# Kernel optimization log

Measured on AMD Instinct MI355X. Metric: run time of the kernel, lower is better.

## Reference

```python
import jax, jax.numpy as jnp
import numpy as np

B, N_ELEM, N_NODES, E2 = 4096, 2048, 1024, 4096


def setup_inputs() -> dict:
    key = jax.random.key(0)
    k = jax.random.split(key, 7)
    return {
        "EA": jax.random.normal(k[0], (B, N_ELEM), dtype=jnp.float32),
        "e": jax.random.normal(k[1], (B, N_ELEM), dtype=jnp.float32),
        "q": jax.random.normal(k[2], (B, N_NODES, 2), dtype=jnp.float32),
        "r": jax.random.normal(k[3], (B, N_NODES, 2), dtype=jnp.float32),
        "vecs": jax.random.normal(k[4], (E2, 2), dtype=jnp.float32),
        "node_ids": jax.random.randint(k[5], (E2,), 0, N_NODES, dtype=jnp.int32),
        "elem_ids": jax.random.randint(k[6], (E2,), 0, N_ELEM, dtype=jnp.int32),
    }


def reference(EA, e, q, r, vecs, node_ids, elem_ids):
    # axial_forces = EA * e : [B, N_ELEM]
    axial = EA * e
    # gather per incidence entry and scale by the 2-vector: [B, E2, 2]
    contrib = axial[:, elem_ids][..., None] * vecs[None, :, :]
    n_sample, n_nodes = q.shape[0], q.shape[1]
    # scatter-add contributions into per-node residual: [B, N_NODES, 2]
    residual = jnp.zeros((n_sample, n_nodes, 2), dtype=EA.dtype)
    residual = residual.at[:, node_ids, :].add(contrib)
    residual = residual - q - r
    return jnp.mean(jnp.square(residual))
```

## Files before the change

kernel.cpp:

```cpp
#include <hip/hip_runtime.h>

#define B_SAMPLES 4096
#define N_ELEM    2048
#define N_NODES   1024
#define E2        4096
#define BLOCK     256
#define MBLOCK    512
#define SLOTS     32
#define S         4
#define MAIN_BLOCKS (B_SAMPLES / S)

#define WS_CNT_OFF   0
#define WS_ELL_OFF   4096
#define WS_PART_OFF  (4096 + SLOTS * N_NODES * 16)

__global__ __launch_bounds__(BLOCK) void neq_zero_kernel(
    float4* __restrict__ ell, int* __restrict__ cnt)
{
    const int i = blockIdx.x * BLOCK + threadIdx.x;
    ell[i] = make_float4(0.f, 0.f, 0.f, 0.f);
    if (i < N_NODES) cnt[i] = 0;
}

__global__ __launch_bounds__(BLOCK) void neq_build_kernel(
    const float* __restrict__ vecs, const int* __restrict__ node_ids,
    const int* __restrict__ elem_ids, int* __restrict__ cnt,
    float4* __restrict__ ell)
{
    const int j = blockIdx.x * BLOCK + threadIdx.x;
    int nid = node_ids[j];
    int eid = elem_ids[j];
    float2 v = ((const float2*)vecs)[j];
    int slot = atomicAdd(&cnt[nid], 1);
    if (slot < SLOTS) {
        ell[slot * N_NODES + nid] = make_float4(v.x, v.y, __int_as_float(eid), 0.f);
    }
}

__global__ __launch_bounds__(MBLOCK, 8) void neq_main_kernel(
    const float* __restrict__ EA, const float* __restrict__ e,
    const float* __restrict__ q,  const float* __restrict__ r,
    const int* __restrict__ cnt, const float4* __restrict__ ell,
    float* __restrict__ partial)
{
    __shared__ float4 axial4[N_ELEM];
    __shared__ float red[MBLOCK / 64];

    const int b0 = blockIdx.x * S;
    const int t = threadIdx.x;

#pragma unroll
    for (int i = 0; i < N_ELEM / MBLOCK; ++i) {
        int eid = t + i * MBLOCK;
        float4 p;
        const float* EAp = EA + (size_t)b0 * N_ELEM + eid;
        const float* ep  = e  + (size_t)b0 * N_ELEM + eid;
        p.x = EAp[0 * N_ELEM] * ep[0 * N_ELEM];
        p.y = EAp[1 * N_ELEM] * ep[1 * N_ELEM];
        p.z = EAp[2 * N_ELEM] * ep[2 * N_ELEM];
        p.w = EAp[3 * N_ELEM] * ep[3 * N_ELEM];
        axial4[eid] = p;
    }

    int c0 = min(cnt[t], SLOTS);
    int c1 = min(cnt[t + MBLOCK], SLOTS);
    int kmax = max(c0, c1);
    __syncthreads();

    float accx[2][S] = {};
    float accy[2][S] = {};
    for (int k = 0; k < kmax; ++k) {
        const float4* row = ell + k * N_NODES + t;
#pragma unroll
        for (int i = 0; i < 2; ++i) {
            float4 pk = row[i * MBLOCK];
            int eid = __float_as_int(pk.z);
            float4 ax = axial4[eid];
            accx[i][0] += ax.x * pk.x;  accy[i][0] += ax.x * pk.y;
            accx[i][1] += ax.y * pk.x;  accy[i][1] += ax.y * pk.y;
            accx[i][2] += ax.z * pk.x;  accy[i][2] += ax.z * pk.y;
            accx[i][3] += ax.w * pk.x;  accy[i][3] += ax.w * pk.y;
        }
    }

    float acc = 0.f;
#pragma unroll
    for (int s = 0; s < S; ++s) {
        const float2* q2 = (const float2*)(q + (size_t)(b0 + s) * N_NODES * 2);
        const float2* r2 = (const float2*)(r + (size_t)(b0 + s) * N_NODES * 2);
#pragma unroll
        for (int i = 0; i < 2; ++i) {
            int n = t + i * MBLOCK;
            float2 qv = q2[n];
            float2 rv = r2[n];
            float x = accx[i][s] - qv.x - rv.x;
            float y = accy[i][s] - qv.y - rv.y;
            acc += x * x + y * y;
        }
    }

#pragma unroll
    for (int off = 32; off > 0; off >>= 1)
        acc += __shfl_down(acc, off, 64);
    if ((t & 63) == 0) red[t >> 6] = acc;
    __syncthreads();
    if (t == 0) {
        float s = 0.f;
#pragma unroll
        for (int w = 0; w < MBLOCK / 64; ++w) s += red[w];
        partial[blockIdx.x] = s;
    }
}

__global__ __launch_bounds__(1024) void neq_reduce_kernel(
    const float* __restrict__ partial, float* __restrict__ out)
{
    __shared__ float red[1024 / 64];
    const int t = threadIdx.x;
    float acc = partial[t];
#pragma unroll
    for (int off = 32; off > 0; off >>= 1)
        acc += __shfl_down(acc, off, 64);
    if ((t & 63) == 0) red[t >> 6] = acc;
    __syncthreads();
    if (t == 0) {
        float s = 0.f;
#pragma unroll
        for (int w = 0; w < 1024 / 64; ++w) s += red[w];
        const float inv_n = 1.0f / (float)((size_t)B_SAMPLES * N_NODES * 2);
        out[0] = s * inv_n;
    }
}

extern "C" void kernel_launch(void* const* d_in, const int* in_sizes, int n_in,
                              void* d_out, int out_size, void* d_ws, size_t ws_size,
                              hipStream_t stream) {
    const float* EA       = (const float*)d_in[0];
    const float* e        = (const float*)d_in[1];
    const float* q        = (const float*)d_in[2];
    const float* r        = (const float*)d_in[3];
    const float* vecs     = (const float*)d_in[4];
    const int*   node_ids = (const int*)d_in[5];
    const int*   elem_ids = (const int*)d_in[6];

    char* ws = (char*)d_ws;
    int*    cnt     = (int*)(ws + WS_CNT_OFF);
    float4* ell     = (float4*)(ws + WS_ELL_OFF);
    float*  partial = (float*)(ws + WS_PART_OFF);

    neq_zero_kernel<<<(SLOTS * N_NODES) / BLOCK, BLOCK, 0, stream>>>(ell, cnt);
    neq_build_kernel<<<E2 / BLOCK, BLOCK, 0, stream>>>(
        vecs, node_ids, elem_ids, cnt, ell);
    neq_main_kernel<<<MAIN_BLOCKS, MBLOCK, 0, stream>>>(
        EA, e, q, r, cnt, ell, partial);
    neq_reduce_kernel<<<1, 1024, 0, stream>>>(partial, (float*)d_out);
}
```

Baseline: 162.4 us.

## Halve samples per block, use float4 loads and swizzled float2 shared axial layout

The main kernel now processes 2 samples per block with 256 threads, so there are twice as many blocks, and each thread handles 4 nodes. EA and e are loaded with vectorized float4 reads. The axial values are stored in shared memory as float2 under a swizzled element index, which the build kernel precomputes so the gather maps correctly. This aims to improve global load coalescing, halve shared memory per block and raise occupancy, at the cost of reading the ELL table twice as many times in total.

```diff
diff --git a/kernel.cpp b/kernel.cpp
--- a/kernel.cpp
+++ b/kernel.cpp
@@ -5,14 +5,18 @@
 #define N_NODES   1024
 #define E2        4096
 #define BLOCK     256
-#define MBLOCK    512
+#define MBLOCK    256
 #define SLOTS     32
-#define S         4
+#define S         2
 #define MAIN_BLOCKS (B_SAMPLES / S)
 
 #define WS_CNT_OFF   0
 #define WS_ELL_OFF   4096
 #define WS_PART_OFF  (4096 + SLOTS * N_NODES * 16)
+
+__host__ __device__ __forceinline__ int swz_eid(int eid) {
+    return ((eid & 3) << 9) | (eid >> 2);
+}
 
 __global__ __launch_bounds__(BLOCK) void neq_zero_kernel(
     float4* __restrict__ ell, int* __restrict__ cnt)
@@ -29,7 +33,7 @@
 {
     const int j = blockIdx.x * BLOCK + threadIdx.x;
     int nid = node_ids[j];
-    int eid = elem_ids[j];
+    int eid = swz_eid(elem_ids[j]);
     float2 v = ((const float2*)vecs)[j];
     int slot = atomicAdd(&cnt[nid], 1);
     if (slot < SLOTS) {
@@ -37,50 +41,75 @@
     }
 }
 
+#define GFMA2(ACCX, ACCY, PK) do { \
+    float2 gv = axial2[__float_as_int((PK).z)]; \
+    (ACCX).x += gv.x * (PK).x; (ACCX).y += gv.y * (PK).x; \
+    (ACCY).x += gv.x * (PK).y; (ACCY).y += gv.y * (PK).y; } while (0)
+
 __global__ __launch_bounds__(MBLOCK, 8) void neq_main_kernel(
     const float* __restrict__ EA, const float* __restrict__ e,
     const float* __restrict__ q,  const float* __restrict__ r,
     const int* __restrict__ cnt, const float4* __restrict__ ell,
     float* __restrict__ partial)
 {
-    __shared__ float4 axial4[N_ELEM];
+    __shared__ float2 axial2[N_ELEM];
     __shared__ float red[MBLOCK / 64];
 
     const int b0 = blockIdx.x * S;
     const int t = threadIdx.x;
 
-#pragma unroll
-    for (int i = 0; i < N_ELEM / MBLOCK; ++i) {
-        int eid = t + i * MBLOCK;
-        float4 p;
-        const float* EAp = EA + (size_t)b0 * N_ELEM + eid;
-        const float* ep  = e  + (size_t)b0 * N_ELEM + eid;
-        p.x = EAp[0 * N_ELEM] * ep[0 * N_ELEM];
-        p.y = EAp[1 * N_ELEM] * ep[1 * N_ELEM];
-        p.z = EAp[2 * N_ELEM] * ep[2 * N_ELEM];
-        p.w = EAp[3 * N_ELEM] * ep[3 * N_ELEM];
-        axial4[eid] = p;
+    const float4* EA4 = (const float4*)(EA + (size_t)b0 * N_ELEM);
+    const float4* e4  = (const float4*)(e  + (size_t)b0 * N_ELEM);
+    float4 a00 = EA4[t];
+    float4 a01 = EA4[t + 256];
+    float4 a10 = EA4[512 + t];
+    float4 a11 = EA4[512 + t + 256];
+    float4 m00 = e4[t];
+    float4 m01 = e4[t + 256];
+    float4 m10 = e4[512 + t];
+    float4 m11 = e4[512 + t + 256];
+
+    int n0 = min(cnt[t], SLOTS);
+    int n1 = min(cnt[t + 256], SLOTS);
+    int n2 = min(cnt[t + 512], SLOTS);
+    int n3 = min(cnt[t + 768], SLOTS);
+    int kmax = max(max(n0, n1), max(n2, n3));
+
+    {
+        float4 p0, p1;
+        p0.x = a00.x * m00.x; p0.y = a00.y * m00.y; p0.z = a00.z * m00.z; p0.w = a00.w * m00.w;
+        p1.x = a10.x * m10.x; p1.y = a10.y * m10.y; p1.z = a10.z * m10.z; p1.w = a10.w * m10.w;
+        axial2[t]        = make_float2(p0.x, p1.x);
+        axial2[t + 512]  = make_float2(p0.y, p1.y);
+        axial2[t + 1024] = make_float2(p0.z, p1.z);
+        axial2[t + 1536] = make_float2(p0.w, p1.w);
     }
-
-    int c0 = min(cnt[t], SLOTS);
-    int c1 = min(cnt[t + MBLOCK], SLOTS);
-    int kmax = max(c0, c1);
+    {
+        float4 p0, p1;
+        p0.x = a01.x * m01.x; p0.y = a01.y * m01.y; p0.z = a01.z * m01.z; p0.w = a01.w * m01.w;
+        p1.x = a11.x * m11.x; p1.y = a11.y * m11.y; p1.z = a11.z * m11.z; p1.w = a11.w * m11.w;
+        axial2[t + 256]  = make_float2(p0.x, p1.x);
+        axial2[t + 768]  = make_float2(p0.y, p1.y);
+        axial2[t + 1280] = make_float2(p0.z, p1.z);
+        axial2[t + 1792] = make_float2(p0.w, p1.w);
+    }
     __syncthreads();
 
-    float accx[2][S] = {};
-    float accy[2][S] = {};
+    float2 accx0 = make_float2(0.f, 0.f), accy0 = make_float2(0.f, 0.f);
+    float2 accx1 = make_float2(0.f, 0.f), accy1 = make_float2(0.f, 0.f);
+    float2 accx2 = make_float2(0.f, 0.f), accy2 = make_float2(0.f, 0.f);
+    float2 accx3 = make_float2(0.f, 0.f), accy3 = make_float2(0.f, 0.f);
+
     for (int k = 0; k < kmax; ++k) {
-        const float4* row = ell + k * N_NODES + t;
-#pragma unroll
-        for (int i = 0; i < 2; ++i) {
-            float4 pk = row[i * MBLOCK];
-            int eid = __float_as_int(pk.z);
-            float4 ax = axial4[eid];
-            accx[i][0] += ax.x * pk.x;  accy[i][0] += ax.x * pk.y;
-            accx[i][1] += ax.y * pk.x;  accy[i][1] += ax.y * pk.y;
-            accx[i][2] += ax.z * pk.x;  accy[i][2] += ax.z * pk.y;
-            accx[i][3] += ax.w * pk.x;  accy[i][3] += ax.w * pk.y;
-        }
+        const float4* row = ell + (size_t)k * N_NODES;
+        float4 pk0 = row[t];
+        float4 pk1 = row[t + 256];
+        float4 pk2 = row[t + 512];
+        float4 pk3 = row[t + 768];
+        GFMA2(accx0, accy0, pk0);
+        GFMA2(accx1, accy1, pk1);
+        GFMA2(accx2, accy2, pk2);
+        GFMA2(accx3, accy3, pk3);
     }
 
     float acc = 0.f;
@@ -88,15 +117,19 @@
     for (int s = 0; s < S; ++s) {
         const float2* q2 = (const float2*)(q + (size_t)(b0 + s) * N_NODES * 2);
         const float2* r2 = (const float2*)(r + (size_t)(b0 + s) * N_NODES * 2);
-#pragma unroll
-        for (int i = 0; i < 2; ++i) {
-            int n = t + i * MBLOCK;
-            float2 qv = q2[n];
-            float2 rv = r2[n];
-            float x = accx[i][s] - qv.x - rv.x;
-            float y = accy[i][s] - qv.y - rv.y;
-            acc += x * x + y * y;
-        }
+        float2 qa = q2[t],       ra = r2[t];
+        float2 qb = q2[t + 256], rb = r2[t + 256];
+        float2 qc = q2[t + 512], rc = r2[t + 512];
+        float2 qd = q2[t + 768], rd = r2[t + 768];
+        float ax, ay, x, y;
+        ax = (s == 0) ? accx0.x : accx0.y;  ay = (s == 0) ? accy0.x : accy0.y;
+        x = ax - qa.x - ra.x;  y = ay - qa.y - ra.y;  acc += x * x + y * y;
+        ax = (s == 0) ? accx1.x : accx1.y;  ay = (s == 0) ? accy1.x : accy1.y;
+        x = ax - qb.x - rb.x;  y = ay - qb.y - rb.y;  acc += x * x + y * y;
+        ax = (s == 0) ? accx2.x : accx2.y;  ay = (s == 0) ? accy2.x : accy2.y;
+        x = ax - qc.x - rc.x;  y = ay - qc.y - rc.y;  acc += x * x + y * y;
+        ax = (s == 0) ? accx3.x : accx3.y;  ay = (s == 0) ? accy3.x : accy3.y;
+        x = ax - qd.x - rd.x;  y = ay - qd.y - rd.y;  acc += x * x + y * y;
     }
 
 #pragma unroll
@@ -104,12 +137,7 @@
         acc += __shfl_down(acc, off, 64);
     if ((t & 63) == 0) red[t >> 6] = acc;
     __syncthreads();
-    if (t == 0) {
-        float s = 0.f;
-#pragma unroll
-        for (int w = 0; w < MBLOCK / 64; ++w) s += red[w];
-        partial[blockIdx.x] = s;
-    }
+    if (t == 0) partial[blockIdx.x] = red[0] + red[1] + red[2] + red[3];
 }
 
 __global__ __launch_bounds__(1024) void neq_reduce_kernel(
@@ -117,7 +145,7 @@
 {
     __shared__ float red[1024 / 64];
     const int t = threadIdx.x;
-    float acc = partial[t];
+    float acc = partial[t] + partial[t + 1024];
 #pragma unroll
     for (int off = 32; off > 0; off >>= 1)
         acc += __shfl_down(acc, off, 64);
```

Result: slower. 192.1 us (+18.3%).

## Process eight samples per block with swizzled axial layout and split ELL arrays

Applied to the files above, without the earlier changes.

Each block now handles eight samples instead of four, so every gathered ELL entry (weight and element index) is reused across twice as many samples. Axial forces are loaded as float4 vectors from global memory and stored transposed into two shared arrays, using a swizzled element index precomputed in the build kernel. The ELL table is split into a float2 weight array and an int index array to cut the bytes read per entry. In exchange, shared memory per block doubles to 64KB and the launch-bounds occupancy hint drops from 8 to 4, which lowers occupancy.

```diff
diff --git a/kernel.cpp b/kernel.cpp
--- a/kernel.cpp
+++ b/kernel.cpp
@@ -7,96 +7,166 @@
 #define BLOCK     256
 #define MBLOCK    512
 #define SLOTS     32
-#define S         4
+#define S         8
 #define MAIN_BLOCKS (B_SAMPLES / S)
 
-#define WS_CNT_OFF   0
-#define WS_ELL_OFF   4096
-#define WS_PART_OFF  (4096 + SLOTS * N_NODES * 16)
+#define WS_CNT_OFF    0
+#define WS_ELLW_OFF   4096
+#define WS_ELLID_OFF  (4096 + SLOTS * N_NODES * 8)
+#define WS_PART_OFF   (WS_ELLID_OFF + SLOTS * N_NODES * 4)
+
+__host__ __device__ __forceinline__ int swz_eid(int eid) {
+    return ((eid & 3) << 9) | (eid >> 2);
+}
 
 __global__ __launch_bounds__(BLOCK) void neq_zero_kernel(
-    float4* __restrict__ ell, int* __restrict__ cnt)
+    float2* __restrict__ ellw, int* __restrict__ ellid, int* __restrict__ cnt)
 {
     const int i = blockIdx.x * BLOCK + threadIdx.x;
-    ell[i] = make_float4(0.f, 0.f, 0.f, 0.f);
+    ellw[i] = make_float2(0.f, 0.f);
+    ellid[i] = 0;
     if (i < N_NODES) cnt[i] = 0;
 }
 
 __global__ __launch_bounds__(BLOCK) void neq_build_kernel(
     const float* __restrict__ vecs, const int* __restrict__ node_ids,
     const int* __restrict__ elem_ids, int* __restrict__ cnt,
-    float4* __restrict__ ell)
+    float2* __restrict__ ellw, int* __restrict__ ellid)
 {
     const int j = blockIdx.x * BLOCK + threadIdx.x;
     int nid = node_ids[j];
-    int eid = elem_ids[j];
+    int sid = swz_eid(elem_ids[j]);
     float2 v = ((const float2*)vecs)[j];
     int slot = atomicAdd(&cnt[nid], 1);
     if (slot < SLOTS) {
-        ell[slot * N_NODES + nid] = make_float4(v.x, v.y, __int_as_float(eid), 0.f);
-    }
-}
-
-__global__ __launch_bounds__(MBLOCK, 8) void neq_main_kernel(
+        ellw[slot * N_NODES + nid] = v;
+        ellid[slot * N_NODES + nid] = sid;
+    }
+}
+
+#define FMA4(A, V, W) do { (A).x += (V).x * (W); (A).y += (V).y * (W); \
+                           (A).z += (V).z * (W); (A).w += (V).w * (W); } while (0)
+
+__global__ __launch_bounds__(MBLOCK, 4) void neq_main_kernel(
     const float* __restrict__ EA, const float* __restrict__ e,
     const float* __restrict__ q,  const float* __restrict__ r,
-    const int* __restrict__ cnt, const float4* __restrict__ ell,
-    float* __restrict__ partial)
-{
-    __shared__ float4 axial4[N_ELEM];
+    const int* __restrict__ cnt, const float2* __restrict__ ellw,
+    const int* __restrict__ ellid, float* __restrict__ partial)
+{
+    __shared__ float4 axialA[N_ELEM];
+    __shared__ float4 axialB[N_ELEM];
     __shared__ float red[MBLOCK / 64];
 
     const int b0 = blockIdx.x * S;
     const int t = threadIdx.x;
 
-#pragma unroll
-    for (int i = 0; i < N_ELEM / MBLOCK; ++i) {
-        int eid = t + i * MBLOCK;
-        float4 p;
-        const float* EAp = EA + (size_t)b0 * N_ELEM + eid;
-        const float* ep  = e  + (size_t)b0 * N_ELEM + eid;
-        p.x = EAp[0 * N_ELEM] * ep[0 * N_ELEM];
-        p.y = EAp[1 * N_ELEM] * ep[1 * N_ELEM];
-        p.z = EAp[2 * N_ELEM] * ep[2 * N_ELEM];
-        p.w = EAp[3 * N_ELEM] * ep[3 * N_ELEM];
-        axial4[eid] = p;
-    }
-
-    int c0 = min(cnt[t], SLOTS);
-    int c1 = min(cnt[t + MBLOCK], SLOTS);
-    int kmax = max(c0, c1);
+    const float4* EA4 = (const float4*)(EA + (size_t)b0 * N_ELEM);
+    const float4* e4  = (const float4*)(e  + (size_t)b0 * N_ELEM);
+    float4 ea0 = EA4[0 * 512 + t];
+    float4 ea1 = EA4[1 * 512 + t];
+    float4 ea2 = EA4[2 * 512 + t];
+    float4 ea3 = EA4[3 * 512 + t];
+    float4 me0 = e4 [0 * 512 + t];
+    float4 me1 = e4 [1 * 512 + t];
+    float4 me2 = e4 [2 * 512 + t];
+    float4 me3 = e4 [3 * 512 + t];
+
+    int c0n = min(cnt[t], SLOTS);
+    int c1n = min(cnt[t + 512], SLOTS);
+    int kmax = max(c0n, c1n);
+
+    {
+        float4 p0, p1, p2, p3;
+        p0.x = ea0.x * me0.x; p0.y = ea0.y * me0.y; p0.z = ea0.z * me0.z; p0.w = ea0.w * me0.w;
+        p1.x = ea1.x * me1.x; p1.y = ea1.y * me1.y; p1.z = ea1.z * me1.z; p1.w = ea1.w * me1.w;
+        p2.x = ea2.x * me2.x; p2.y = ea2.y * me2.y; p2.z = ea2.z * me2.z; p2.w = ea2.w * me2.w;
+        p3.x = ea3.x * me3.x; p3.y = ea3.y * me3.y; p3.z = ea3.z * me3.z; p3.w = ea3.w * me3.w;
+        axialA[t]        = make_float4(p0.x, p1.x, p2.x, p3.x);
+        axialA[512 + t]  = make_float4(p0.y, p1.y, p2.y, p3.y);
+        axialA[1024 + t] = make_float4(p0.z, p1.z, p2.z, p3.z);
+        axialA[1536 + t] = make_float4(p0.w, p1.w, p2.w, p3.w);
+    }
+    {
+        float4 fa0 = EA4[4 * 512 + t];
+        float4 fa1 = EA4[5 * 512 + t];
+        float4 fa2 = EA4[6 * 512 + t];
+        float4 fa3 = EA4[7 * 512 + t];
+        float4 fm0 = e4 [4 * 512 + t];
+        float4 fm1 = e4 [5 * 512 + t];
+        float4 fm2 = e4 [6 * 512 + t];
+        float4 fm3 = e4 [7 * 512 + t];
+        float4 p0, p1, p2, p3;
+        p0.x = fa0.x * fm0.x; p0.y = fa0.y * fm0.y; p0.z = fa0.z * fm0.z; p0.w = fa0.w * fm0.w;
+        p1.x = fa1.x * fm1.x; p1.y = fa1.y * fm1.y; p1.z = fa1.z * fm1.z; p1.w = fa1.w * fm1.w;
+        p2.x = fa2.x * fm2.x; p2.y = fa2.y * fm2.y; p2.z = fa2.z * fm2.z; p2.w = fa2.w * fm2.w;
+        p3.x = fa3.x * fm3.x; p3.y = fa3.y * fm3.y; p3.z = fa3.z * fm3.z; p3.w = fa3.w * fm3.w;
+        axialB[t]        = make_float4(p0.x, p1.x, p2.x, p3.x);
+        axialB[512 + t]  = make_float4(p0.y, p1.y, p2.y, p3.y);
+        axialB[1024 + t] = make_float4(p0.z, p1.z, p2.z, p3.z);
+        axialB[1536 + t] = make_float4(p0.w, p1.w, p2.w, p3.w);
+    }
     __syncthreads();
 
-    float accx[2][S] = {};
-    float accy[2][S] = {};
+    float4 xA0 = make_float4(0.f, 0.f, 0.f, 0.f);
+    float4 yA0 = make_float4(0.f, 0.f, 0.f, 0.f);
+    float4 xB0 = make_float4(0.f, 0.f, 0.f, 0.f);
+    float4 yB0 = make_float4(0.f, 0.f, 0.f, 0.f);
+    float4 xA1 = make_float4(0.f, 0.f, 0.f, 0.f);
+    float4 yA1 = make_float4(0.f, 0.f, 0.f, 0.f);
+    float4 xB1 = make_float4(0.f, 0.f, 0.f, 0.f);
+    float4 yB1 = make_float4(0.f, 0.f, 0.f, 0.f);
+
     for (int k = 0; k < kmax; ++k) {
-        const float4* row = ell + k * N_NODES + t;
-#pragma unroll
-        for (int i = 0; i < 2; ++i) {
-            float4 pk = row[i * MBLOCK];
-            int eid = __float_as_int(pk.z);
-            float4 ax = axial4[eid];
-            accx[i][0] += ax.x * pk.x;  accy[i][0] += ax.x * pk.y;
-            accx[i][1] += ax.y * pk.x;  accy[i][1] += ax.y * pk.y;
-            accx[i][2] += ax.z * pk.x;  accy[i][2] += ax.z * pk.y;
-            accx[i][3] += ax.w * pk.x;  accy[i][3] += ax.w * pk.y;
-        }
+        const float2* rw  = ellw  + (size_t)k * N_NODES;
+        const int*    rid = ellid + (size_t)k * N_NODES;
+        float2 w0 = rw[t];
+        float2 w1 = rw[t + 512];
+        int i0 = rid[t];
+        int i1 = rid[t + 512];
+        float4 A0 = axialA[i0];
+        float4 B0 = axialB[i0];
+        float4 A1 = axialA[i1];
+        float4 B1 = axialB[i1];
+        FMA4(xA0, A0, w0.x);  FMA4(yA0, A0, w0.y);
+        FMA4(xB0, B0, w0.x);  FMA4(yB0, B0, w0.y);
+        FMA4(xA1, A1, w1.x);  FMA4(yA1, A1, w1.y);
+        FMA4(xB1, B1, w1.x);  FMA4(yB1, B1, w1.y);
     }
 
     float acc = 0.f;
 #pragma unroll
-    for (int s = 0; s < S; ++s) {
+    for (int s = 0; s < 4; ++s) {
         const float2* q2 = (const float2*)(q + (size_t)(b0 + s) * N_NODES * 2);
         const float2* r2 = (const float2*)(r + (size_t)(b0 + s) * N_NODES * 2);
-#pragma unroll
-        for (int i = 0; i < 2; ++i) {
-            int n = t + i * MBLOCK;
-            float2 qv = q2[n];
-            float2 rv = r2[n];
-            float x = accx[i][s] - qv.x - rv.x;
-            float y = accy[i][s] - qv.y - rv.y;
-            acc += x * x + y * y;
-        }
+        float2 qa = q2[t],       ra = r2[t];
+        float2 qb = q2[t + 512], rb = r2[t + 512];
+        float ax0 = (s == 0) ? xA0.x : (s == 1) ? xA0.y : (s == 2) ? xA0.z : xA0.w;
+        float ay0 = (s == 0) ? yA0.x : (s == 1) ? yA0.y : (s == 2) ? yA0.z : yA0.w;
+        float ax1 = (s == 0) ? xA1.x : (s == 1) ? xA1.y : (s == 2) ? xA1.z : xA1.w;
+        float ay1 = (s == 0) ? yA1.x : (s == 1) ? yA1.y : (s == 2) ? yA1.z : yA1.w;
+        float x = ax0 - qa.x - ra.x;
+        float y = ay0 - qa.y - ra.y;
+        acc += x * x + y * y;
+        x = ax1 - qb.x - rb.x;
+        y = ay1 - qb.y - rb.y;
+        acc += x * x + y * y;
+    }
+#pragma unroll
+    for (int s = 0; s < 4; ++s) {
+        const float2* q2 = (const float2*)(q + (size_t)(b0 + 4 + s) * N_NODES * 2);
+        const float2* r2 = (const float2*)(r + (size_t)(b0 + 4 + s) * N_NODES * 2);
+        float2 qa = q2[t],       ra = r2[t];
+        float2 qb = q2[t + 512], rb = r2[t + 512];
+        float ax0 = (s == 0) ? xB0.x : (s == 1) ? xB0.y : (s == 2) ? xB0.z : xB0.w;
+        float ay0 = (s == 0) ? yB0.x : (s == 1) ? yB0.y : (s == 2) ? yB0.z : yB0.w;
+        float ax1 = (s == 0) ? xB1.x : (s == 1) ? xB1.y : (s == 2) ? xB1.z : xB1.w;
+        float ay1 = (s == 0) ? yB1.x : (s == 1) ? yB1.y : (s == 2) ? yB1.z : yB1.w;
+        float x = ax0 - qa.x - ra.x;
+        float y = ay0 - qa.y - ra.y;
+        acc += x * x + y * y;
+        x = ax1 - qb.x - rb.x;
+        y = ay1 - qb.y - rb.y;
+        acc += x * x + y * y;
     }
 
 #pragma unroll
@@ -112,10 +182,10 @@
     }
 }
 
-__global__ __launch_bounds__(1024) void neq_reduce_kernel(
+__global__ __launch_bounds__(512) void neq_reduce_kernel(
     const float* __restrict__ partial, float* __restrict__ out)
 {
-    __shared__ float red[1024 / 64];
+    __shared__ float red[512 / 64];
     const int t = threadIdx.x;
     float acc = partial[t];
 #pragma unroll
@@ -126,7 +196,7 @@
     if (t == 0) {
         float s = 0.f;
 #pragma unroll
-        for (int w = 0; w < 1024 / 64; ++w) s += red[w];
+        for (int w = 0; w < 512 / 64; ++w) s += red[w];
         const float inv_n = 1.0f / (float)((size_t)B_SAMPLES * N_NODES * 2);
         out[0] = s * inv_n;
     }
@@ -145,13 +215,14 @@
 
     char* ws = (char*)d_ws;
     int*    cnt     = (int*)(ws + WS_CNT_OFF);
-    float4* ell     = (float4*)(ws + WS_ELL_OFF);
+    float2* ellw    = (float2*)(ws + WS_ELLW_OFF);
+    int*    ellid   = (int*)(ws + WS_ELLID_OFF);
     float*  partial = (float*)(ws + WS_PART_OFF);
 
-    neq_zero_kernel<<<(SLOTS * N_NODES) / BLOCK, BLOCK, 0, stream>>>(ell, cnt);
+    neq_zero_kernel<<<(SLOTS * N_NODES) / BLOCK, BLOCK, 0, stream>>>(ellw, ellid, cnt);
     neq_build_kernel<<<E2 / BLOCK, BLOCK, 0, stream>>>(
-        vecs, node_ids, elem_ids, cnt, ell);
+        vecs, node_ids, elem_ids, cnt, ellw, ellid);
     neq_main_kernel<<<MAIN_BLOCKS, MBLOCK, 0, stream>>>(
-        EA, e, q, r, cnt, ell, partial);
-    neq_reduce_kernel<<<1, 1024, 0, stream>>>(partial, (float*)d_out);
-}
+        EA, e, q, r, cnt, ellw, ellid, partial);
+    neq_reduce_kernel<<<1, 512, 0, stream>>>(partial, (float*)d_out);
+}
```

Measured after the change: 163.3 us. About the same (+0.5%).
